# Optimization experiments

Measured on AMD Instinct MI355X. Metric: run time of the kernel, lower is better.

The kernel has to match this reference:

```python
import jax, jax.numpy as jnp
import numpy as np

B, N, E = 128, 196, 2048   # batch, num_features (14x14), encoder_dim
D, A = 512, 512            # decoder_dim, attention_dim


def setup_inputs() -> dict:
    key = jax.random.key(0)
    ks = jax.random.split(key, 8)
    s_e = 1.0 / np.sqrt(E)
    s_d = 1.0 / np.sqrt(D)
    s_a = 1.0 / np.sqrt(A)
    return {
        "encoder_out": jax.random.normal(ks[0], (B, N, E), dtype=jnp.float32),
        "decoder_hidden": jax.random.normal(ks[1], (B, D), dtype=jnp.float32),
        "We": jax.random.uniform(ks[2], (E, A), jnp.float32, -s_e, s_e),
        "be": jax.random.uniform(ks[3], (A,), jnp.float32, -s_e, s_e),
        "Wd": jax.random.uniform(ks[4], (D, A), jnp.float32, -s_d, s_d),
        "bd": jax.random.uniform(ks[5], (A,), jnp.float32, -s_d, s_d),
        "Wf": jax.random.uniform(ks[6], (A, 1), jnp.float32, -s_a, s_a),
        "bf": jax.random.uniform(ks[7], (1,), jnp.float32, -s_a, s_a),
    }


def reference(encoder_out, decoder_hidden, We, be, Wd, bd, Wf, bf):
    # att1: [B,N,A] projection of encoder features
    att1 = jnp.einsum('bne,ea->bna', encoder_out, We) + be
    # att2: [B,A] projection of decoder state, broadcast over N
    att2 = decoder_hidden @ Wd + bd
    att = jnp.tanh(att1 + att2[:, None, :])          # [B,N,A]
    scores = jnp.einsum('bna,ao->bno', att, Wf) + bf  # [B,N,1]
    alpha = jax.nn.softmax(scores, axis=1)            # softmax over num_features
    context = jnp.sum(encoder_out * alpha, axis=1)    # [B,E]
    return (context, alpha)
```

## Files before the change

kernel.cpp:

```cpp
#include <hip/hip_runtime.h>
#include <hip/hip_bf16.h>
#include <stdint.h>

#define B_   128
#define N_   196
#define E_   2048
#define D_   512
#define A_   512
#define MTOT (B_ * N_)

typedef short  short8  __attribute__((ext_vector_type(8)));
typedef float  floatx4 __attribute__((ext_vector_type(4)));

__device__ __forceinline__ unsigned short f2bf(float f) {
    union { float f; uint32_t u; } v; v.f = f;
    uint32_t r = v.u + 0x7FFFu + ((v.u >> 16) & 1u);
    return (unsigned short)(r >> 16);
}

__device__ __forceinline__ uint32_t pkbf(float a, float b) {
    uint32_t ua = __float_as_uint(a) + 0x8000u;
    uint32_t ub = __float_as_uint(b) + 0x8000u;
    return __builtin_amdgcn_perm(ub, ua, 0x07060302u);
}

__global__ void transcvt_k(const float* __restrict__ We, unsigned short* __restrict__ WeT) {
    __shared__ float tile[32][33];
    const int e0 = blockIdx.x * 32, a0 = blockIdx.y * 32;
    const int t = threadIdx.x, tc = t & 31, tr = t >> 5;
#pragma unroll
    for (int i = 0; i < 4; ++i) {
        int r = tr + i * 8;
        tile[r][tc] = We[(size_t)(e0 + r) * A_ + a0 + tc];
    }
    __syncthreads();
#pragma unroll
    for (int i = 0; i < 4; ++i) {
        int r = tr + i * 8;
        WeT[(size_t)(a0 + r) * E_ + e0 + tc] = f2bf(tile[tc][r]);
    }
}

__launch_bounds__(512)
__global__ void att2_k(const float* __restrict__ dh, const float* __restrict__ Wd,
                       const float* __restrict__ bd, const float* __restrict__ be,
                       float* __restrict__ att2p) {
    const int b = blockIdx.x, t = threadIdx.x;
    __shared__ float sdh[D_];
    sdh[t] = dh[b * D_ + t];
    __syncthreads();
    float acc = 0.f;
#pragma unroll 8
    for (int d = 0; d < D_; ++d) acc += sdh[d] * Wd[(size_t)d * A_ + t];
    att2p[(size_t)b * A_ + t] = acc + bd[t] + be[t];
}

__launch_bounds__(256, 3)
__global__ void score_gemm(const float* __restrict__ enc,
                           const unsigned short* __restrict__ WeT,
                           const float* __restrict__ att2p,
                           const float* __restrict__ Wf,
                           float* __restrict__ scoresP) {
    __shared__ __align__(16) char sMem[16384 + 8192];
    __shared__ float sPart[4][64];

    const int t   = threadIdx.x;
    const int w   = t >> 6;
    const int l   = t & 63;
    const int l15 = l & 15;
    const int q4  = l >> 4;
    const int wm  = w >> 1;
    const int wn  = w & 1;
    const int row0 = blockIdx.y * 128;
    const int col0 = blockIdx.x * 128;

    floatx4 acc[4][4] = {};

    const float* aSrc[4];
    int aDst[4];
#pragma unroll
    for (int j = 0; j < 4; ++j) {
        int s  = w * 256 + j * 64 + l;
        int r  = s >> 3, p = s & 7;
        int cs = p ^ (r & 7);
        aSrc[j] = enc + (size_t)(row0 + r) * E_ + cs * 4;
        aDst[j] = (w * 256 + j * 64) * 16;
    }
    const unsigned short* bSrc[2];
    int bDst[2];
#pragma unroll
    for (int j = 0; j < 2; ++j) {
        int s  = w * 128 + j * 64 + l;
        int n  = s >> 2, p = s & 3;
        int cs = p ^ ((n >> 2) & 3);
        bSrc[j] = WeT + (size_t)(col0 + n) * E_ + cs * 8;
        bDst[j] = 16384 + (w * 128 + j * 64) * 16;
    }

    const int p0 = (2 * q4) ^ (l15 & 7);
    int offA[4], offA2[4], offB[4];
#pragma unroll
    for (int mi = 0; mi < 4; ++mi) {
        int rA  = wm * 64 + mi * 16 + l15;
        offA[mi]  = rA * 128 + p0 * 16;
        offA2[mi] = rA * 128 + (p0 ^ 1) * 16;
    }
#pragma unroll
    for (int ni = 0; ni < 4; ++ni) {
        int nB = wn * 64 + ni * 16 + l15;
        offB[ni] = 16384 + nB * 64 + (q4 ^ ((l15 >> 2) & 3)) * 16;
    }

    for (int kk = 0; kk < 64; ++kk) {
#pragma unroll
        for (int j = 0; j < 4; ++j)
            __builtin_amdgcn_global_load_lds(
                (const __attribute__((address_space(1))) uint32_t*)(aSrc[j] + kk * 32),
                (__attribute__((address_space(3))) uint32_t*)(sMem + aDst[j]), 16, 0, 0);
#pragma unroll
        for (int j = 0; j < 2; ++j)
            __builtin_amdgcn_global_load_lds(
                (const __attribute__((address_space(1))) uint32_t*)(bSrc[j] + kk * 32),
                (__attribute__((address_space(3))) uint32_t*)(sMem + bDst[j]), 16, 0, 0);
        __syncthreads();

        short8 bfr[4];
        union { uint32_t u[4]; short8 s; } af[4];
#pragma unroll
        for (int ni = 0; ni < 4; ++ni)
            bfr[ni] = *(const short8*)(sMem + offB[ni]);
#pragma unroll
        for (int mi = 0; mi < 4; ++mi) {
            float4 lo = *(const float4*)(sMem + offA[mi]);
            float4 hi = *(const float4*)(sMem + offA2[mi]);
            af[mi].u[0] = pkbf(lo.x, lo.y);
            af[mi].u[1] = pkbf(lo.z, lo.w);
            af[mi].u[2] = pkbf(hi.x, hi.y);
            af[mi].u[3] = pkbf(hi.z, hi.w);
        }
#pragma unroll
        for (int mi = 0; mi < 4; ++mi) {
            acc[mi][0] = __builtin_amdgcn_mfma_f32_16x16x32_bf16(af[mi].s, bfr[0], acc[mi][0], 0, 0, 0);
            acc[mi][1] = __builtin_amdgcn_mfma_f32_16x16x32_bf16(af[mi].s, bfr[1], acc[mi][1], 0, 0, 0);
            acc[mi][2] = __builtin_amdgcn_mfma_f32_16x16x32_bf16(af[mi].s, bfr[2], acc[mi][2], 0, 0, 0);
            acc[mi][3] = __builtin_amdgcn_mfma_f32_16x16x32_bf16(af[mi].s, bfr[3], acc[mi][3], 0, 0, 0);
        }
        __syncthreads();
    }

    const int cbase = col0 + wn * 64;
    float wfv[4];
#pragma unroll
    for (int ni = 0; ni < 4; ++ni) wfv[ni] = Wf[cbase + ni * 16 + l15];

#pragma unroll
    for (int mi = 0; mi < 4; ++mi) {
#pragma unroll
        for (int r = 0; r < 4; ++r) {
            const int m    = mi * 16 + q4 * 4 + r;
            const int grow = row0 + wm * 64 + m;
            const int bb   = grow / N_;
            const float* a2 = att2p + (size_t)bb * A_ + cbase;
            float s = 0.f;
#pragma unroll
            for (int ni = 0; ni < 4; ++ni) {
                float v  = acc[mi][ni][r] + a2[ni * 16 + l15];
                float e  = __expf(2.f * v);
                float th = 1.f - 2.f / (e + 1.f);
                s += th * wfv[ni];
            }
            s += __shfl_xor(s, 1);
            s += __shfl_xor(s, 2);
            s += __shfl_xor(s, 4);
            s += __shfl_xor(s, 8);
            if (l15 == 0) sPart[w][m] = s;
        }
    }
    __syncthreads();
    if (t < 128) {
        const int h = t >> 6, m = t & 63;
        float v = sPart[h * 2 + 0][m] + sPart[h * 2 + 1][m];
        scoresP[(size_t)blockIdx.x * MTOT + row0 + t] = v;
    }
}

__global__ void softmax_k(const float* __restrict__ sp, float* __restrict__ alpha) {
    const int b = blockIdx.x, t = threadIdx.x;
    const int w = t >> 6, l = t & 63;
    __shared__ float red[8];
    float v = -3.0e38f;
    if (t < N_) v = sp[b * N_ + t] + sp[MTOT + b * N_ + t]
                  + sp[2 * MTOT + b * N_ + t] + sp[3 * MTOT + b * N_ + t];
    float m = v;
#pragma unroll
    for (int off = 32; off >= 1; off >>= 1) m = fmaxf(m, __shfl_xor(m, off));
    if (l == 0) red[w] = m;
    __syncthreads();
    m = fmaxf(fmaxf(red[0], red[1]), fmaxf(red[2], red[3]));
    float e = 0.f;
    if (t < N_) e = __expf(v - m);
    float s = e;
#pragma unroll
    for (int off = 32; off >= 1; off >>= 1) s += __shfl_xor(s, off);
    if (l == 0) red[4 + w] = s;
    __syncthreads();
    s = red[4] + red[5] + red[6] + red[7];
    if (t < N_) alpha[b * N_ + t] = e / s;
}

__launch_bounds__(256)
__global__ void context_k(const float* __restrict__ enc, const float* __restrict__ alpha,
                          float* __restrict__ ctx) {
    const int chunk = blockIdx.x, b = blockIdx.y;
    const int t = threadIdx.x, tn = t >> 6, tc = t & 63;
    __shared__ float  sAl[N_];
    __shared__ float4 sRed[256];
    if (t < N_) sAl[t] = alpha[b * N_ + t];
    __syncthreads();
    const float* base = enc + (size_t)b * N_ * E_ + chunk * 256 + tc * 4;
    float4 a = make_float4(0.f, 0.f, 0.f, 0.f);
#pragma unroll 7
    for (int n = tn; n < N_; n += 4) {
        float  al = sAl[n];
        float4 v  = *(const float4*)(base + (size_t)n * E_);
        a.x += al * v.x; a.y += al * v.y; a.z += al * v.z; a.w += al * v.w;
    }
    sRed[t] = a;
    __syncthreads();
    if (t < 64) {
        float4 r0 = sRed[t], r1 = sRed[t + 64], r2 = sRed[t + 128], r3 = sRed[t + 192];
        float4 o = make_float4(r0.x + r1.x + r2.x + r3.x, r0.y + r1.y + r2.y + r3.y,
                               r0.z + r1.z + r2.z + r3.z, r0.w + r1.w + r2.w + r3.w);
        *(float4*)(ctx + (size_t)b * E_ + chunk * 256 + t * 4) = o;
    }
}

extern "C" void kernel_launch(void* const* d_in, const int* in_sizes, int n_in,
                              void* d_out, int out_size, void* d_ws, size_t ws_size,
                              hipStream_t stream) {
    const float* enc = (const float*)d_in[0];
    const float* dh  = (const float*)d_in[1];
    const float* We  = (const float*)d_in[2];
    const float* be  = (const float*)d_in[3];
    const float* Wd  = (const float*)d_in[4];
    const float* bd  = (const float*)d_in[5];
    const float* Wf  = (const float*)d_in[6];

    float* out   = (float*)d_out;
    float* ctx   = out;
    float* alpha = out + B_ * E_;

    char* ws = (char*)d_ws;
    unsigned short* WeT  = (unsigned short*)ws;
    float* att2p         = (float*)(ws + (2u << 20));
    float* scoresP       = (float*)(ws + (2u << 20) + (256u << 10));

    transcvt_k <<<dim3(E_ / 32, A_ / 32), 256, 0, stream>>>(We, WeT);
    att2_k     <<<dim3(B_),              512, 0, stream>>>(dh, Wd, bd, be, att2p);
    score_gemm <<<dim3(4, MTOT / 128),   256, 0, stream>>>(enc, WeT, att2p, Wf, scoresP);
    softmax_k  <<<dim3(B_),              256, 0, stream>>>(scoresP, alpha);
    context_k  <<<dim3(E_ / 256, B_),    256, 0, stream>>>(enc, alpha, ctx);
}
```

Measured before the change: 495.6 us.

## Retile score GEMM to 64x512 per block so encoder rows load once

The score GEMM now uses 512-thread blocks that each own 64 rows and the full 512-column attention dimension. Previously there were 128x128 tiles across 4 column blocks, so each fp32 encoder row was read from global memory four times. The new tiling reads each row once, and the score partials are reduced inside the block instead of across four partial buffers, which also simplifies softmax. The cost is more LDS per block (40KB) and a larger share of traffic spent on WeT tiles per row, since every block now streams the whole bf16 weight matrix.

```diff
diff --git a/kernel.cpp b/kernel.cpp
--- a/kernel.cpp
+++ b/kernel.cpp
@@ -55,70 +55,54 @@
     att2p[(size_t)b * A_ + t] = acc + bd[t] + be[t];
 }
 
-__launch_bounds__(256, 3)
+__launch_bounds__(512, 4)
 __global__ void score_gemm(const float* __restrict__ enc,
                            const unsigned short* __restrict__ WeT,
                            const float* __restrict__ att2p,
                            const float* __restrict__ Wf,
                            float* __restrict__ scoresP) {
-    __shared__ __align__(16) char sMem[16384 + 8192];
-    __shared__ float sPart[4][64];
+    __shared__ __align__(16) char sMem[8192 + 32768];
+    __shared__ float sPart[8][64];
 
     const int t   = threadIdx.x;
     const int w   = t >> 6;
     const int l   = t & 63;
     const int l15 = l & 15;
     const int q4  = l >> 4;
-    const int wm  = w >> 1;
-    const int wn  = w & 1;
-    const int row0 = blockIdx.y * 128;
-    const int col0 = blockIdx.x * 128;
+    const int row0 = blockIdx.x * 64;
 
     floatx4 acc[4][4] = {};
 
-    const float* aSrc[4];
-    int aDst[4];
+    const float* aSrc;
+    int aDst;
+    {
+        int s = w * 64 + l;
+        int r = s >> 3, p = s & 7;
+        aSrc = enc + (size_t)(row0 + r) * E_ + ((p ^ (r & 7)) * 4);
+        aDst = w * 1024;
+    }
+    const unsigned short* bSrc[4];
+    int bDst[4];
 #pragma unroll
     for (int j = 0; j < 4; ++j) {
-        int s  = w * 256 + j * 64 + l;
-        int r  = s >> 3, p = s & 7;
-        int cs = p ^ (r & 7);
-        aSrc[j] = enc + (size_t)(row0 + r) * E_ + cs * 4;
-        aDst[j] = (w * 256 + j * 64) * 16;
-    }
-    const unsigned short* bSrc[2];
-    int bDst[2];
-#pragma unroll
-    for (int j = 0; j < 2; ++j) {
-        int s  = w * 128 + j * 64 + l;
-        int n  = s >> 2, p = s & 3;
-        int cs = p ^ ((n >> 2) & 3);
-        bSrc[j] = WeT + (size_t)(col0 + n) * E_ + cs * 8;
-        bDst[j] = 16384 + (w * 128 + j * 64) * 16;
-    }
-
-    const int p0 = (2 * q4) ^ (l15 & 7);
-    int offA[4], offA2[4], offB[4];
-#pragma unroll
-    for (int mi = 0; mi < 4; ++mi) {
-        int rA  = wm * 64 + mi * 16 + l15;
-        offA[mi]  = rA * 128 + p0 * 16;
-        offA2[mi] = rA * 128 + (p0 ^ 1) * 16;
-    }
-#pragma unroll
-    for (int ni = 0; ni < 4; ++ni) {
-        int nB = wn * 64 + ni * 16 + l15;
-        offB[ni] = 16384 + nB * 64 + (q4 ^ ((l15 >> 2) & 3)) * 16;
-    }
+        int s = (w * 4 + j) * 64 + l;
+        int n = s >> 2, p = s & 3;
+        int q = p ^ ((n >> 1) & 3);
+        bSrc[j] = WeT + (size_t)n * E_ + q * 8;
+        bDst[j] = 8192 + (w * 4 + j) * 1024;
+    }
+
+    const int pLo   = (2 * q4) ^ (l15 & 7);
+    const int offAlo = l15 * 128 + pLo * 16;
+    const int offAhi = l15 * 128 + (pLo ^ 1) * 16;
+    const int offB   = 8192 + (w * 64 + l15) * 64 + (q4 ^ ((l15 >> 1) & 3)) * 16;
 
     for (int kk = 0; kk < 64; ++kk) {
+        __builtin_amdgcn_global_load_lds(
+            (const __attribute__((address_space(1))) uint32_t*)(aSrc + kk * 32),
+            (__attribute__((address_space(3))) uint32_t*)(sMem + aDst), 16, 0, 0);
 #pragma unroll
         for (int j = 0; j < 4; ++j)
-            __builtin_amdgcn_global_load_lds(
-                (const __attribute__((address_space(1))) uint32_t*)(aSrc[j] + kk * 32),
-                (__attribute__((address_space(3))) uint32_t*)(sMem + aDst[j]), 16, 0, 0);
-#pragma unroll
-        for (int j = 0; j < 2; ++j)
             __builtin_amdgcn_global_load_lds(
                 (const __attribute__((address_space(1))) uint32_t*)(bSrc[j] + kk * 32),
                 (__attribute__((address_space(3))) uint32_t*)(sMem + bDst[j]), 16, 0, 0);
@@ -128,11 +112,11 @@
         union { uint32_t u[4]; short8 s; } af[4];
 #pragma unroll
         for (int ni = 0; ni < 4; ++ni)
-            bfr[ni] = *(const short8*)(sMem + offB[ni]);
+            bfr[ni] = *(const short8*)(sMem + offB + ni * 1024);
 #pragma unroll
         for (int mi = 0; mi < 4; ++mi) {
-            float4 lo = *(const float4*)(sMem + offA[mi]);
-            float4 hi = *(const float4*)(sMem + offA2[mi]);
+            float4 lo = *(const float4*)(sMem + offAlo + mi * 2048);
+            float4 hi = *(const float4*)(sMem + offAhi + mi * 2048);
             af[mi].u[0] = pkbf(lo.x, lo.y);
             af[mi].u[1] = pkbf(lo.z, lo.w);
             af[mi].u[2] = pkbf(hi.x, hi.y);
@@ -148,7 +132,7 @@
         __syncthreads();
     }
 
-    const int cbase = col0 + wn * 64;
+    const int cbase = w * 64;
     float wfv[4];
 #pragma unroll
     for (int ni = 0; ni < 4; ++ni) wfv[ni] = Wf[cbase + ni * 16 + l15];
@@ -158,7 +142,7 @@
 #pragma unroll
         for (int r = 0; r < 4; ++r) {
             const int m    = mi * 16 + q4 * 4 + r;
-            const int grow = row0 + wm * 64 + m;
+            const int grow = row0 + m;
             const int bb   = grow / N_;
             const float* a2 = att2p + (size_t)bb * A_ + cbase;
             float s = 0.f;
@@ -177,10 +161,11 @@
         }
     }
     __syncthreads();
-    if (t < 128) {
-        const int h = t >> 6, m = t & 63;
-        float v = sPart[h * 2 + 0][m] + sPart[h * 2 + 1][m];
-        scoresP[(size_t)blockIdx.x * MTOT + row0 + t] = v;
+    if (t < 64) {
+        float v = 0.f;
+#pragma unroll
+        for (int ww = 0; ww < 8; ++ww) v += sPart[ww][t];
+        scoresP[row0 + t] = v;
     }
 }
 
@@ -189,8 +174,7 @@
     const int w = t >> 6, l = t & 63;
     __shared__ float red[8];
     float v = -3.0e38f;
-    if (t < N_) v = sp[b * N_ + t] + sp[MTOT + b * N_ + t]
-                  + sp[2 * MTOT + b * N_ + t] + sp[3 * MTOT + b * N_ + t];
+    if (t < N_) v = sp[b * N_ + t];
     float m = v;
 #pragma unroll
     for (int off = 32; off >= 1; off >>= 1) m = fmaxf(m, __shfl_xor(m, off));
@@ -257,7 +241,7 @@
 
     transcvt_k <<<dim3(E_ / 32, A_ / 32), 256, 0, stream>>>(We, WeT);
     att2_k     <<<dim3(B_),              512, 0, stream>>>(dh, Wd, bd, be, att2p);
-    score_gemm <<<dim3(4, MTOT / 128),   256, 0, stream>>>(enc, WeT, att2p, Wf, scoresP);
+    score_gemm <<<dim3(MTOT / 64),       512, 0, stream>>>(enc, WeT, att2p, Wf, scoresP);
     softmax_k  <<<dim3(B_),              256, 0, stream>>>(scoresP, alpha);
     context_k  <<<dim3(E_ / 256, B_),    256, 0, stream>>>(enc, alpha, ctx);
 }
```

After: 440.0 us. 1.13x faster.
